# Kernel optimization log

Measured on AMD Instinct MI355X. Metric: run time of the kernel, lower is better.

The kernel has to match this reference:

```python
import jax, jax.numpy as jnp
import numpy as np

H = 128  # hidden/input size fixed by module


def setup_inputs() -> dict:
    key = jax.random.key(0)
    ks = jax.random.split(key, 8)
    S, B = 512, 256
    scale = 1.0 / np.sqrt(H)
    return {
        "X": jax.random.normal(ks[0], (S, B, H), dtype=jnp.float32),
        "h": jax.random.normal(ks[1], (1, B, H), dtype=jnp.float32),
        "lin_W": jax.random.uniform(ks[2], (H, H), jnp.float32, -scale, scale),
        "lin_b": jax.random.uniform(ks[3], (H,), jnp.float32, -scale, scale),
        "W_ih": jax.random.uniform(ks[4], (3 * H, H), jnp.float32, -scale, scale),
        "W_hh": jax.random.uniform(ks[5], (3 * H, H), jnp.float32, -scale, scale),
        "b_ih": jax.random.uniform(ks[6], (3 * H,), jnp.float32, -scale, scale),
        "b_hh": jax.random.uniform(ks[7], (3 * H,), jnp.float32, -scale, scale),
    }


def reference(X, h, lin_W, lin_b, W_ih, W_hh, b_ih, b_hh):
    # Linear: y = X @ W^T + b   (torch nn.Linear convention)
    Xp = jnp.einsum("sbd,ed->sbe", X, lin_W) + lin_b
    # Precompute input-hidden gate projections for all timesteps: (S, B, 3H)
    gx_all = jnp.einsum("sbd,gd->sbg", Xp, W_ih) + b_ih

    def step(h_t, gx):
        gh = h_t @ W_hh.T + b_hh  # (B, 3H)
        xr, xz, xn = jnp.split(gx, 3, axis=-1)
        hr, hz, hn = jnp.split(gh, 3, axis=-1)
        r = jax.nn.sigmoid(xr + hr)
        z = jax.nn.sigmoid(xz + hz)
        n = jnp.tanh(xn + r * hn)
        h_new = (1.0 - z) * n + z * h_t
        return h_new, h_new

    _, outs = jax.lax.scan(step, h[0], gx_all)
    return outs  # (S, B, H) — the module returns only the output sequence
```

## Files before the change

### kernel.cpp

```cpp
#include <hip/hip_runtime.h>
#include <math.h>

#define HID 128
#define G3  384
#define BATCH 256
#define SEQ 512
#define NB 16
#define NBLK (BATCH/NB)
#define NB4 4
#define NBLK4 (BATCH/NB4)

typedef __bf16 bf16x8 __attribute__((ext_vector_type(8)));
typedef __bf16 bf16x4 __attribute__((ext_vector_type(4)));
typedef float  f32x4  __attribute__((ext_vector_type(4)));

#define LOG2E 1.44269504088896f
#define SC_RZ (-1.44269504088896f)
#define SC_N  (-2.88539008177793f)

__device__ __forceinline__ float sigm(float x) {
    return __builtin_amdgcn_rcpf(1.f + __builtin_amdgcn_exp2f(-LOG2E * x));
}
__device__ __forceinline__ float tanh_fast(float x) {
    float e = __builtin_amdgcn_exp2f(-2.f * LOG2E * x);
    return __builtin_amdgcn_rcpf(1.f + e) * 2.f - 1.f;
}
__device__ __forceinline__ f32x4 mfma16(bf16x8 a, bf16x8 b, f32x4 c) {
    return __builtin_amdgcn_mfma_f32_16x16x32_bf16(a, b, c, 0, 0, 0);
}
__device__ __forceinline__ bf16x8 cvt8(float4 a, float4 b) {
    bf16x8 f;
    f[0] = (__bf16)a.x; f[1] = (__bf16)a.y; f[2] = (__bf16)a.z; f[3] = (__bf16)a.w;
    f[4] = (__bf16)b.x; f[5] = (__bf16)b.y; f[6] = (__bf16)b.z; f[7] = (__bf16)b.w;
    return f;
}
__device__ __forceinline__ bf16x8 cvt8s(float4 a, float4 b, float s) {
    bf16x8 f;
    f[0] = (__bf16)(a.x*s); f[1] = (__bf16)(a.y*s); f[2] = (__bf16)(a.z*s); f[3] = (__bf16)(a.w*s);
    f[4] = (__bf16)(b.x*s); f[5] = (__bf16)(b.y*s); f[6] = (__bf16)(b.z*s); f[7] = (__bf16)(b.w*s);
    return f;
}
__device__ __forceinline__ bf16x4 cvt4(float4 a) {
    bf16x4 f;
    f[0] = (__bf16)a.x; f[1] = (__bf16)a.y; f[2] = (__bf16)a.z; f[3] = (__bf16)a.w;
    return f;
}


__global__ void fold_bf16_kernel(const float* __restrict__ lin_W,
                                 const float* __restrict__ lin_b,
                                 const float* __restrict__ W_ih,
                                 const float* __restrict__ b_ih,
                                 __bf16* __restrict__ Wcbf,
                                 float* __restrict__ bcA) {
    const int g = blockIdx.x;
    const int d = threadIdx.x;
    const float sc = (g < 2 * HID) ? SC_RZ : SC_N;
    float acc = 0.f;
    #pragma unroll 16
    for (int e = 0; e < HID; ++e) acc += W_ih[g * HID + e] * lin_W[e * HID + d];
    Wcbf[g * HID + d] = (__bf16)(acc * sc);
    if (d == 0) {
        float b = 0.f;
        for (int e = 0; e < HID; ++e) b += W_ih[g * HID + e] * lin_b[e];
        bcA[g] = (b + b_ih[g]) * sc;
    }
}

#define GEMM_TILE(MT, CUR, NXT)                                               \
  {                                                                           \
    int mtn_ = (MT) + 1; if (mtn_ > 7) mtn_ = 7;                              \
    const float* pxn_ = X + (size_t)(m0 + mtn_ * 16 + col) * HID + lr * 8;    \
    _Pragma("unroll")                                                         \
    for (int kt = 0; kt < 4; ++kt) {                                          \
        NXT[2 * kt]     = *(const float4*)(pxn_ + kt * 32);                   \
        NXT[2 * kt + 1] = *(const float4*)(pxn_ + kt * 32 + 4);               \
    }                                                                         \
    bf16x8 Bx_[4];                                                            \
    _Pragma("unroll")                                                         \
    for (int kt = 0; kt < 4; ++kt) Bx_[kt] = cvt8(CUR[2 * kt], CUR[2 * kt + 1]); \
    const int m_ = m0 + (MT) * 16 + col;                                      \
    _Pragma("unroll")                                                         \
    for (int j = 0; j < 6; ++j) {                                             \
        f32x4 acc_ = vb[j];                                                   \
        acc_ = mfma16(A[j][0], Bx_[0], acc_);                                 \
        acc_ = mfma16(A[j][1], Bx_[1], acc_);                                 \
        acc_ = mfma16(A[j][2], Bx_[2], acc_);                                 \
        acc_ = mfma16(A[j][3], Bx_[3], acc_);                                 \
        float4 o_; o_.x = acc_[0]; o_.y = acc_[1]; o_.z = acc_[2]; o_.w = acc_[3]; \
        *(bf16x4*)(gx + (size_t)m_ * G3 + (w * 6 + j) * 16 + lr * 4) = cvt4(o_); \
    }                                                                         \
  }

__global__ __launch_bounds__(256, 2)
void gemm_gx2(const float* __restrict__ X,
              const __bf16* __restrict__ Wcbf,
              const float* __restrict__ bcA,
              __bf16* __restrict__ gx) {
    const int t   = threadIdx.x;
    const int w   = t >> 6;
    const int l   = t & 63;
    const int col = l & 15;
    const int lr  = l >> 4;
    const int m0  = blockIdx.x * 128;

    bf16x8 A[6][4];
    #pragma unroll
    for (int j = 0; j < 6; ++j)
        #pragma unroll
        for (int kt = 0; kt < 4; ++kt)
            A[j][kt] = *(const bf16x8*)(Wcbf +
                (size_t)((w * 6 + j) * 16 + col) * HID + kt * 32 + lr * 8);
    #pragma unroll
    for (int j = 0; j < 6; ++j)
        #pragma unroll
        for (int kt = 0; kt < 4; ++kt)
            asm volatile("" : "+v"(A[j][kt]));

    f32x4 vb[6];
    #pragma unroll
    for (int j = 0; j < 6; ++j)
        vb[j] = *(const f32x4*)(bcA + (w * 6 + j) * 16 + lr * 4);

    float4 xe[8], xo[8];
    {
        const float* px = X + (size_t)(m0 + col) * HID + lr * 8;
        #pragma unroll
        for (int kt = 0; kt < 4; ++kt) {
            xe[2 * kt]     = *(const float4*)(px + kt * 32);
            xe[2 * kt + 1] = *(const float4*)(px + kt * 32 + 4);
        }
    }
    for (int mt = 0; mt < 8; mt += 2) {
        GEMM_TILE(mt,     xe, xo);
        GEMM_TILE(mt + 1, xo, xe);
    }
}

#define SPLIT_STEP(S, C0, C1, C2, N0, N1, N2)                                 \
  {                                                                           \
               \
    bf16x8 Bh_[4];                                                            \
    _Pragma("unroll")                                                         \
    for (int kt = 0; kt < 4; ++kt)                                            \
        Bh_[kt] = *(const bf16x8*)(hbuf + SW(col, kt * 64 + lr * 16));        \
    f32x4 ar_ = vbr, az_ = vbz, anh_ = vbnh;                                  \
    _Pragma("unroll")                                                         \
    for (int kt = 0; kt < 4; ++kt) {                                          \
        ar_  = mfma16(aW[0][kt], Bh_[kt], ar_);                               \
        az_  = mfma16(aW[1][kt], Bh_[kt], az_);                               \
        anh_ = mfma16(aW[2][kt], Bh_[kt], anh_);                              \
    }                                                                         \
    if (col < NB4) {                                                          \
        float* gp_ = ghsF + col * 388 + w * 16 + lr * 4;                      \
        *(f32x4*)(gp_)       = ar_;                                           \
        *(f32x4*)(gp_ + 128) = az_;                                           \
        *(f32x4*)(gp_ + 256) = anh_;                                          \
    }                                                                         \
    asm volatile("s_waitcnt lgkmcnt(0)" ::: "memory");                        \
    __builtin_amdgcn_s_barrier();                                             \
                      \
    int sp_ = (S) + 1; if (sp_ > SEQ - 1) sp_ = SEQ - 1;                      \
    const __bf16* p_ = gx + (size_t)sp_ * (BATCH * G3) + gxoff;               \
    asm volatile("global_load_ushort %0, %3, off\n\t"                         \
                 "global_load_ushort %1, %3, off offset:256\n\t"              \
                 "global_load_ushort %2, %3, off offset:512"                  \
                 : "=&v"(N0), "=&v"(N1), "=&v"(N2) : "v"(p_) : "memory");     \
    float gr_ = ghsF[bi * 388 + ri];                                          \
    float gz_ = ghsF[bi * 388 + 128 + ri];                                    \
    float gn_ = ghsF[bi * 388 + 256 + ri];                                    \
                                      \
    asm volatile("s_waitcnt vmcnt(4)" ::: "memory");                          \
    __builtin_amdgcn_sched_barrier(0);                                        \
    float xr_ = __uint_as_float((C0) << 16);                                  \
    float xz_ = __uint_as_float((C1) << 16);                                  \
    float xn_ = __uint_as_float((C2) << 16);                                  \
    float r_ = __builtin_amdgcn_rcpf(1.f + __builtin_amdgcn_exp2f(gr_ + xr_));\
    float z_ = __builtin_amdgcn_rcpf(1.f + __builtin_amdgcn_exp2f(gz_ + xz_));\
    float n_ = 2.f * __builtin_amdgcn_rcpf(1.f + __builtin_amdgcn_exp2f(xn_ + r_ * gn_)) - 1.f; \
    float hn_ = n_ + z_ * (hold - n_);                                        \
    hold = hn_;                                                               \
    *(__bf16*)(hbuf + SW(bi, ri * 2)) = (__bf16)hn_;                          \
    out[((size_t)(S) * BATCH + bb + bi) * HID + ri] = hn_;                    \
    asm volatile("s_waitcnt lgkmcnt(0)" ::: "memory");                        \
    __builtin_amdgcn_s_barrier();                                             \
  }

__global__ __launch_bounds__(512, 2)
void gru_scan_split(const float* __restrict__ h0,
                    const float* __restrict__ W_hh,
                    const float* __restrict__ b_hh,
                    const __bf16* __restrict__ gx,
                    float* __restrict__ out) {
    const int t   = threadIdx.x;
    const int w   = t >> 6;
    const int l   = t & 63;
    const int col = l & 15;
    const int lr  = l >> 4;
    const int bb  = blockIdx.x * NB4;
    const int bi  = t >> 7;
    const int ri  = t & 127;

    __shared__ __align__(16) unsigned char lds[4096 + 4 * 388 * 4];
    unsigned char* hbuf = lds;
    float* ghsF = (float*)(lds + 4096);

    auto SW = [](int b, int off) { return b * 256 + (off ^ ((b & 7) << 4)); };

    bf16x8 aW[3][4];
    #pragma unroll
    for (int g3 = 0; g3 < 3; ++g3) {
        const float s = (g3 < 2) ? SC_RZ : SC_N;
        #pragma unroll
        for (int kt = 0; kt < 4; ++kt) {
            const int row = g3 * HID + w * 16 + col;
            const float* pw = W_hh + row * HID + kt * 32 + lr * 8;
            aW[g3][kt] = cvt8s(*(const float4*)pw, *(const float4*)(pw + 4), s);
        }
    }
    #pragma unroll
    for (int g3 = 0; g3 < 3; ++g3)
        #pragma unroll
        for (int kt = 0; kt < 4; ++kt)
            asm volatile("" : "+v"(aW[g3][kt]));

    f32x4 vbr, vbz, vbnh;
    #pragma unroll
    for (int q = 0; q < 4; ++q) {
        const int g = w * 16 + lr * 4 + q;
        vbr[q]  = b_hh[g] * SC_RZ;
        vbz[q]  = b_hh[HID + g] * SC_RZ;
        vbnh[q] = b_hh[2 * HID + g] * SC_N;
    }

    float hold = h0[(size_t)(bb + bi) * HID + ri];
    asm volatile("" :: "v"(hold), "v"(vbr), "v"(vbz), "v"(vbnh));

    const size_t gxoff = (size_t)(bb + bi) * G3 + ri;

    if (t < 64) {
        const int sb = t >> 4, k8 = (t & 15) * 8;
        const float* ph = h0 + (size_t)(bb + sb) * HID + k8;
        *(bf16x8*)(hbuf + SW(sb, k8 * 2)) =
            cvt8(*(const float4*)ph, *(const float4*)(ph + 4));
    } else if (t < 256) {
        const int sb = t >> 4, k8 = (t & 15) * 8;
        uint4 z = {0u, 0u, 0u, 0u};
        *(uint4*)(hbuf + SW(sb, k8 * 2)) = z;
    }

    unsigned c0, c1, c2, n0, n1, n2, dm;
    {
        const __bf16* p_ = gx + gxoff;
        asm volatile("global_load_ushort %0, %3, off\n\t"
                     "global_load_ushort %1, %3, off offset:256\n\t"
                     "global_load_ushort %2, %3, off offset:512"
                     : "=&v"(c0), "=&v"(c1), "=&v"(c2) : "v"(p_) : "memory");
        asm volatile("global_load_ushort %0, %1, off"
                     : "=&v"(dm) : "v"(p_) : "memory");
    }
    asm volatile("s_waitcnt lgkmcnt(0)" ::: "memory");
    __builtin_amdgcn_s_barrier();

    for (int s0 = 0; s0 < SEQ; s0 += 2) {
        SPLIT_STEP(s0,     c0, c1, c2, n0, n1, n2);
        SPLIT_STEP(s0 + 1, n0, n1, n2, c0, c1, c2);
    }
    asm volatile("" :: "v"(dm));
}

__global__ void fold_kernel(const float* __restrict__ lin_W,
                            const float* __restrict__ lin_b,
                            const float* __restrict__ W_ih,
                            const float* __restrict__ b_ih,
                            float* __restrict__ Wc,
                            float* __restrict__ bcA) {
    const int g = blockIdx.x;
    const int d = threadIdx.x;
    float acc = 0.f;
    for (int e = 0; e < HID; ++e) acc += W_ih[g * HID + e] * lin_W[e * HID + d];
    Wc[g * HID + d] = acc;
    if (d == 0) {
        float b = 0.f;
        for (int e = 0; e < HID; ++e) b += W_ih[g * HID + e] * lin_b[e];
        bcA[g] = b + b_ih[g];
    }
}

__global__ __launch_bounds__(512, 2)
void gru_scan_mfma(const float* __restrict__ X,
                   const float* __restrict__ h0,
                   const float* __restrict__ W_hh,
                   const float* __restrict__ b_hh,
                   const float* __restrict__ Wc,
                   const float* __restrict__ bcA,
                   float* __restrict__ out) {
    const int t   = threadIdx.x;
    const int w   = t >> 6;
    const int l   = t & 63;
    const int col = l & 15;
    const int lr  = l >> 4;
    const int bb  = blockIdx.x * NB;

    __shared__ __align__(16) unsigned char lds[16384];
    unsigned char* hA = lds;
    unsigned char* hB = lds + 4096;
    unsigned char* xA = lds + 8192;
    unsigned char* xB = lds + 12288;

    auto SW = [](int b, int off) { return b * 256 + (off ^ ((b & 7) << 4)); };

    bf16x8 aW[3][4], aC[3][4];
    #pragma unroll
    for (int g3 = 0; g3 < 3; ++g3)
        #pragma unroll
        for (int kt = 0; kt < 4; ++kt) {
            const int row = g3 * HID + w * 16 + col;
            const float* pw = W_hh + row * HID + kt * 32 + lr * 8;
            const float* pc = Wc   + row * HID + kt * 32 + lr * 8;
            aW[g3][kt] = cvt8(*(const float4*)pw, *(const float4*)(pw + 4));
            aC[g3][kt] = cvt8(*(const float4*)pc, *(const float4*)(pc + 4));
        }
    #pragma unroll
    for (int g3 = 0; g3 < 3; ++g3)
        #pragma unroll
        for (int kt = 0; kt < 4; ++kt) {
            asm volatile("" : "+v"(aW[g3][kt]));
            asm volatile("" : "+v"(aC[g3][kt]));
        }

    f32x4 vbr, vbz, vbnx, vbnh;
    #pragma unroll
    for (int q = 0; q < 4; ++q) {
        const int g = w * 16 + lr * 4 + q;
        vbr[q]  = bcA[g] + b_hh[g];
        vbz[q]  = bcA[HID + g] + b_hh[HID + g];
        vbnx[q] = bcA[2 * HID + g];
        vbnh[q] = b_hh[2 * HID + g];
    }

    f32x4 hold = *(const f32x4*)(h0 + (size_t)(bb + col) * HID + w * 16 + lr * 4);

    const int sb = t >> 5;
    const int sk = (t & 31) * 4;

    float4 xp, xq;
    if (t < 256) {
        const int hb = t >> 4, hk = (t & 15) * 8;
        const float* ph = h0 + (size_t)(bb + hb) * HID + hk;
        *(bf16x8*)(hA + SW(hb, hk * 2)) =
            cvt8(*(const float4*)ph, *(const float4*)(ph + 4));
    }
    {
        const float* px = X + ((size_t)0 * BATCH + bb + sb) * HID + sk;
        *(bf16x4*)(xA + SW(sb, sk * 2)) = cvt4(*(const float4*)px);
        const float* p1 = X + ((size_t)1 * BATCH + bb + sb) * HID + sk;
        xp = *(const float4*)p1;
    }
    asm volatile("s_waitcnt lgkmcnt(0)" ::: "memory");
    __builtin_amdgcn_s_barrier();

    auto STEP = [&](int s, unsigned char* hR, unsigned char* hW,
                    unsigned char* xR, unsigned char* xW,
                    float4& xc, float4& xn) {
        *(bf16x4*)(xW + SW(sb, sk * 2)) = cvt4(xc);
        {
            int sp = s + 2; if (sp > SEQ - 1) sp = SEQ - 1;
            const float* px = X + ((size_t)sp * BATCH + bb + sb) * HID + sk;
            xn = *(const float4*)px;
        }
        bf16x8 Bh[4], Bx[4];
        #pragma unroll
        for (int kt = 0; kt < 4; ++kt) {
            Bh[kt] = *(const bf16x8*)(hR + SW(col, kt * 64 + lr * 16));
            Bx[kt] = *(const bf16x8*)(xR + SW(col, kt * 64 + lr * 16));
        }
        f32x4 ar = vbr, az = vbz, anh = vbnh, anx = vbnx;
        #pragma unroll
        for (int kt = 0; kt < 4; ++kt) {
            ar  = mfma16(aW[0][kt], Bh[kt], ar);
            ar  = mfma16(aC[0][kt], Bx[kt], ar);
            az  = mfma16(aW[1][kt], Bh[kt], az);
            az  = mfma16(aC[1][kt], Bx[kt], az);
            anh = mfma16(aW[2][kt], Bh[kt], anh);
            anx = mfma16(aC[2][kt], Bx[kt], anx);
        }
        f32x4 hnew;
        #pragma unroll
        for (int q = 0; q < 4; ++q) {
            float r = sigm(ar[q]);
            float z = sigm(az[q]);
            float n = tanh_fast(anx[q] + r * anh[q]);
            hnew[q] = n + z * (hold[q] - n);
        }
        hold = hnew;
        *(bf16x4*)(hW + SW(col, (w * 16 + lr * 4) * 2)) = cvt4(*(float4*)&hnew);
        float4 o; o.x = hnew[0]; o.y = hnew[1]; o.z = hnew[2]; o.w = hnew[3];
        *(float4*)(out + ((size_t)s * BATCH + bb + col) * HID + w * 16 + lr * 4) = o;
        asm volatile("s_waitcnt lgkmcnt(0)" ::: "memory");
        __builtin_amdgcn_s_barrier();
    };

    for (int s0 = 0; s0 < SEQ; s0 += 2) {
        STEP(s0,     hA, hB, xA, xB, xp, xq);
        STEP(s0 + 1, hB, hA, xB, xA, xq, xp);
    }
}

extern "C" void kernel_launch(void* const* d_in, const int* in_sizes, int n_in,
                              void* d_out, int out_size, void* d_ws, size_t ws_size,
                              hipStream_t stream) {
    const float* X     = (const float*)d_in[0];
    const float* h0    = (const float*)d_in[1];
    const float* lin_W = (const float*)d_in[2];
    const float* lin_b = (const float*)d_in[3];
    const float* W_ih  = (const float*)d_in[4];
    const float* W_hh  = (const float*)d_in[5];
    const float* b_ih  = (const float*)d_in[6];
    const float* b_hh  = (const float*)d_in[7];
    float* out = (float*)d_out;

    const size_t GX_BYTES   = (size_t)SEQ * BATCH * G3 * 2;
    const size_t WCBF_BYTES = (size_t)G3 * HID * 2;
    const size_t BCA_BYTES  = (size_t)G3 * 4;

    if (ws_size >= GX_BYTES + WCBF_BYTES + BCA_BYTES) {
        __bf16* gxp  = (__bf16*)d_ws;
        __bf16* Wcbf = (__bf16*)((char*)d_ws + GX_BYTES);
        float*  bcA  = (float*)((char*)d_ws + GX_BYTES + WCBF_BYTES);

        fold_bf16_kernel<<<G3, HID, 0, stream>>>(lin_W, lin_b, W_ih, b_ih, Wcbf, bcA);
        gemm_gx2<<<(SEQ * BATCH) / 128, 256, 0, stream>>>(X, Wcbf, bcA, gxp);
        gru_scan_split<<<NBLK4, 512, 0, stream>>>(h0, W_hh, b_hh, gxp, out);
    } else {
        float* Wc  = (float*)d_ws;
        float* bcA = Wc + G3 * HID;
        fold_kernel<<<G3, HID, 0, stream>>>(lin_W, lin_b, W_ih, b_ih, Wc, bcA);
        gru_scan_mfma<<<NBLK, 512, 0, stream>>>(X, h0, W_hh, b_hh, Wc, bcA, out);
    }
}
```

Before: 363.7 us.

## Split GRU scan into 2-batch blocks of 4 waves with dual accumulators

Each GRU scan block now covers 2 batch rows with 256 threads (4 waves) instead of 4 rows with 512 threads. Each wave therefore handles two 16-row gate tiles per gate and holds twice as many W_hh register fragments. The launch grows to 128 blocks, spreading the sequential recurrence over more CUs and cutting per-block barrier participants. Each gate's K reduction is also split across two independent MFMA accumulator chains that are summed at the end, shortening the dependency chain. The cost is more register pressure and a 16-column MFMA tile of which only 2 columns are useful.

```diff
diff --git a/kernel.cpp b/kernel.cpp
--- a/kernel.cpp
+++ b/kernel.cpp
@@ -7,8 +7,9 @@
 #define SEQ 512
 #define NB 16
 #define NBLK (BATCH/NB)
-#define NB4 4
-#define NBLK4 (BATCH/NB4)
+#define NBS 2
+#define NBLKS (BATCH/NBS)
+#define GHP 392
 
 typedef __bf16 bf16x8 __attribute__((ext_vector_type(8)));
 typedef __bf16 bf16x4 __attribute__((ext_vector_type(4)));
@@ -139,23 +140,27 @@
 
 #define SPLIT_STEP(S, C0, C1, C2, N0, N1, N2)                                 \
   {                                                                           \
-               \
+              \
     bf16x8 Bh_[4];                                                            \
     _Pragma("unroll")                                                         \
     for (int kt = 0; kt < 4; ++kt)                                            \
         Bh_[kt] = *(const bf16x8*)(hbuf + SW(col, kt * 64 + lr * 16));        \
-    f32x4 ar_ = vbr, az_ = vbz, anh_ = vbnh;                                  \
     _Pragma("unroll")                                                         \
-    for (int kt = 0; kt < 4; ++kt) {                                          \
-        ar_  = mfma16(aW[0][kt], Bh_[kt], ar_);                               \
-        az_  = mfma16(aW[1][kt], Bh_[kt], az_);                               \
-        anh_ = mfma16(aW[2][kt], Bh_[kt], anh_);                              \
-    }                                                                         \
-    if (col < NB4) {                                                          \
-        float* gp_ = ghsF + col * 388 + w * 16 + lr * 4;                      \
-        *(f32x4*)(gp_)       = ar_;                                           \
-        *(f32x4*)(gp_ + 128) = az_;                                           \
-        *(f32x4*)(gp_ + 256) = anh_;                                          \
+    for (int j = 0; j < 2; ++j) {                                             \
+        _Pragma("unroll")                                                     \
+        for (int g3 = 0; g3 < 3; ++g3) {                                      \
+            f32x4 aA = vb[j][g3];                                             \
+            f32x4 aB = vzero;                                                 \
+            aA = mfma16(aW[j][g3][0], Bh_[0], aA);                            \
+            aB = mfma16(aW[j][g3][1], Bh_[1], aB);                            \
+            aA = mfma16(aW[j][g3][2], Bh_[2], aA);                            \
+            aB = mfma16(aW[j][g3][3], Bh_[3], aB);                            \
+            aA = aA + aB;                                                     \
+            if (col < NBS) {                                                  \
+                float* gp_ = ghsF + col * GHP + g3 * 128 + (2 * w + j) * 16 + lr * 4; \
+                *(f32x4*)(gp_) = aA;                                          \
+            }                                                                 \
+        }                                                                     \
     }                                                                         \
     asm volatile("s_waitcnt lgkmcnt(0)" ::: "memory");                        \
     __builtin_amdgcn_s_barrier();                                             \
@@ -166,10 +171,10 @@
                  "global_load_ushort %1, %3, off offset:256\n\t"              \
                  "global_load_ushort %2, %3, off offset:512"                  \
                  : "=&v"(N0), "=&v"(N1), "=&v"(N2) : "v"(p_) : "memory");     \
-    float gr_ = ghsF[bi * 388 + ri];                                          \
-    float gz_ = ghsF[bi * 388 + 128 + ri];                                    \
-    float gn_ = ghsF[bi * 388 + 256 + ri];                                    \
-                                      \
+    float gr_ = ghsF[bi * GHP + ri];                                          \
+    float gz_ = ghsF[bi * GHP + 128 + ri];                                    \
+    float gn_ = ghsF[bi * GHP + 256 + ri];                                    \
+          \
     asm volatile("s_waitcnt vmcnt(4)" ::: "memory");                          \
     __builtin_amdgcn_sched_barrier(0);                                        \
     float xr_ = __uint_as_float((C0) << 16);                                  \
@@ -186,64 +191,72 @@
     __builtin_amdgcn_s_barrier();                                             \
   }
 
-__global__ __launch_bounds__(512, 2)
-void gru_scan_split(const float* __restrict__ h0,
-                    const float* __restrict__ W_hh,
-                    const float* __restrict__ b_hh,
-                    const __bf16* __restrict__ gx,
-                    float* __restrict__ out) {
+__global__ __launch_bounds__(256, 2)
+void gru_scan_split4w(const float* __restrict__ h0,
+                      const float* __restrict__ W_hh,
+                      const float* __restrict__ b_hh,
+                      const __bf16* __restrict__ gx,
+                      float* __restrict__ out) {
     const int t   = threadIdx.x;
     const int w   = t >> 6;
     const int l   = t & 63;
     const int col = l & 15;
     const int lr  = l >> 4;
-    const int bb  = blockIdx.x * NB4;
+    const int bb  = blockIdx.x * NBS;
     const int bi  = t >> 7;
     const int ri  = t & 127;
 
-    __shared__ __align__(16) unsigned char lds[4096 + 4 * 388 * 4];
+    __shared__ __align__(16) unsigned char lds[4096 + NBS * GHP * 4];
     unsigned char* hbuf = lds;
     float* ghsF = (float*)(lds + 4096);
 
     auto SW = [](int b, int off) { return b * 256 + (off ^ ((b & 7) << 4)); };
 
-    bf16x8 aW[3][4];
-    #pragma unroll
-    for (int g3 = 0; g3 < 3; ++g3) {
-        const float s = (g3 < 2) ? SC_RZ : SC_N;
-        #pragma unroll
-        for (int kt = 0; kt < 4; ++kt) {
-            const int row = g3 * HID + w * 16 + col;
-            const float* pw = W_hh + row * HID + kt * 32 + lr * 8;
-            aW[g3][kt] = cvt8s(*(const float4*)pw, *(const float4*)(pw + 4), s);
-        }
-    }
-    #pragma unroll
-    for (int g3 = 0; g3 < 3; ++g3)
-        #pragma unroll
-        for (int kt = 0; kt < 4; ++kt)
-            asm volatile("" : "+v"(aW[g3][kt]));
-
-    f32x4 vbr, vbz, vbnh;
-    #pragma unroll
-    for (int q = 0; q < 4; ++q) {
-        const int g = w * 16 + lr * 4 + q;
-        vbr[q]  = b_hh[g] * SC_RZ;
-        vbz[q]  = b_hh[HID + g] * SC_RZ;
-        vbnh[q] = b_hh[2 * HID + g] * SC_N;
-    }
+    const f32x4 vzero = {0.f, 0.f, 0.f, 0.f};
+
+    bf16x8 aW[2][3][4];
+    #pragma unroll
+    for (int j = 0; j < 2; ++j)
+        #pragma unroll
+        for (int g3 = 0; g3 < 3; ++g3) {
+            const float s = (g3 < 2) ? SC_RZ : SC_N;
+            #pragma unroll
+            for (int kt = 0; kt < 4; ++kt) {
+                const int row = g3 * HID + (2 * w + j) * 16 + col;
+                const float* pw = W_hh + row * HID + kt * 32 + lr * 8;
+                aW[j][g3][kt] = cvt8s(*(const float4*)pw, *(const float4*)(pw + 4), s);
+            }
+        }
+    #pragma unroll
+    for (int j = 0; j < 2; ++j)
+        #pragma unroll
+        for (int g3 = 0; g3 < 3; ++g3)
+            #pragma unroll
+            for (int kt = 0; kt < 4; ++kt)
+                asm volatile("" : "+v"(aW[j][g3][kt]));
+
+    f32x4 vb[2][3];
+    #pragma unroll
+    for (int j = 0; j < 2; ++j)
+        #pragma unroll
+        for (int q = 0; q < 4; ++q) {
+            const int g = (2 * w + j) * 16 + lr * 4 + q;
+            vb[j][0][q] = b_hh[g] * SC_RZ;
+            vb[j][1][q] = b_hh[HID + g] * SC_RZ;
+            vb[j][2][q] = b_hh[2 * HID + g] * SC_N;
+        }
 
     float hold = h0[(size_t)(bb + bi) * HID + ri];
-    asm volatile("" :: "v"(hold), "v"(vbr), "v"(vbz), "v"(vbnh));
+    asm volatile("" :: "v"(hold));
 
     const size_t gxoff = (size_t)(bb + bi) * G3 + ri;
 
-    if (t < 64) {
+    if (t < 32) {
         const int sb = t >> 4, k8 = (t & 15) * 8;
         const float* ph = h0 + (size_t)(bb + sb) * HID + k8;
         *(bf16x8*)(hbuf + SW(sb, k8 * 2)) =
             cvt8(*(const float4*)ph, *(const float4*)(ph + 4));
-    } else if (t < 256) {
+    } else {
         const int sb = t >> 4, k8 = (t & 15) * 8;
         uint4 z = {0u, 0u, 0u, 0u};
         *(uint4*)(hbuf + SW(sb, k8 * 2)) = z;
@@ -431,7 +444,7 @@
 
         fold_bf16_kernel<<<G3, HID, 0, stream>>>(lin_W, lin_b, W_ih, b_ih, Wcbf, bcA);
         gemm_gx2<<<(SEQ * BATCH) / 128, 256, 0, stream>>>(X, Wcbf, bcA, gxp);
-        gru_scan_split<<<NBLK4, 512, 0, stream>>>(h0, W_hh, b_hh, gxp, out);
+        gru_scan_split4w<<<NBLKS, 256, 0, stream>>>(h0, W_hh, b_hh, gxp, out);
     } else {
         float* Wc  = (float*)d_ws;
         float* bcA = Wc + G3 * HID;
```

After: 364.3 us. No clear change (+0.2%).
